# Optimization experiments

Hardware: AMD Instinct MI355X
Metric: run time of the kernel (lower is better)

The kernel has to match this reference:

```python
import jax, jax.numpy as jnp
import numpy as np

DT = 0.1  # fixed RK4 step size from the constructor

def setup_inputs() -> dict:
    key = jax.random.key(0)
    k1, k2, k3 = jax.random.split(key, 3)
    B, U, H = 65536, 128, 512
    x0 = jax.random.normal(k1, (B, U), dtype=jnp.float32)
    # small init so 20 unrolled RK4 steps stay numerically tame
    W1 = jax.random.normal(k2, (U, H), dtype=jnp.float32) * (0.5 / np.sqrt(U))
    b1 = jnp.zeros((H,), dtype=jnp.float32)
    W2 = jax.random.normal(k3, (H, U), dtype=jnp.float32) * (0.5 / np.sqrt(H))
    b2 = jnp.zeros((U,), dtype=jnp.float32)
    return {"x0": x0, "W1": W1, "b1": b1, "W2": W2, "b2": b2}

def _mlp(x, W1, b1, W2, b2):
    # vector field: Dense(512, relu) -> Dense(128); time-independent
    return jnp.maximum(x @ W1 + b1, 0.0) @ W2 + b2

def _rk4_integrate(x, n_steps, W1, b1, W2, b2):
    def step(x, _):
        k1 = _mlp(x, W1, b1, W2, b2)
        k2 = _mlp(x + 0.5 * DT * k1, W1, b1, W2, b2)
        k3 = _mlp(x + 0.5 * DT * k2, W1, b1, W2, b2)
        k4 = _mlp(x + DT * k3, W1, b1, W2, b2)
        return x + (DT / 6.0) * (k1 + 2.0 * k2 + 2.0 * k3 + k4), None
    x, _ = jax.lax.scan(step, x, None, length=n_steps)
    return x

def reference(x0, W1, b1, W2, b2):
    # phase 1: integrate t in [0, t1/2 = 1.0] -> 10 RK4 steps at dt=0.1
    x = _rk4_integrate(x0, 10, W1, b1, W2, b2)
    # phase 2: n=5 macro-steps of length (1.0 - 0.0)/5 = 0.2 -> 2 RK4 steps each
    def macro(x, _):
        x = _rk4_integrate(x, 2, W1, b1, W2, b2)
        return x, None
    x, _ = jax.lax.scan(macro, x, None, length=5)
    return x
```

## Files before the change

kernel.cpp:

```cpp
#include <hip/hip_runtime.h>
#include <stdint.h>


typedef _Float16 half8 __attribute__((ext_vector_type(8)));
typedef float f32x4 __attribute__((ext_vector_type(4)));
typedef __attribute__((address_space(3))) char lchar;
typedef __attribute__((address_space(1))) char gchar;

#define XSTR 136

static __device__ __forceinline__ void gload_lds16(const void* g, void* l) {
  __builtin_amdgcn_global_load_lds((const gchar*)g, (lchar*)l, 16, 0, 0);
}

static __device__ __forceinline__ unsigned short f2h(float x) {
  union { _Float16 h; unsigned short u; } cv;
  cv.h = (_Float16)x;
  return cv.u;
}
static __device__ __forceinline__ float h2f(unsigned short u) {
  union { unsigned short u; _Float16 h; } cv;
  cv.u = u;
  return (float)cv.h;
}
static __device__ __forceinline__ uint64_t pack4(float a, float b, float c, float d) {
  union { _Float16 h[4]; uint64_t q; } cv;
  cv.h[0] = (_Float16)a; cv.h[1] = (_Float16)b;
  cv.h[2] = (_Float16)c; cv.h[3] = (_Float16)d;
  return cv.q;
}

__global__ void pack_w(const float* __restrict__ W1, const float* __restrict__ W2,
                       unsigned short* __restrict__ wp) {
  int id = blockIdx.x * 256 + threadIdx.x;
  int lane = id & 63, fid = (id >> 6) & 255;
  int g = lane >> 4, lm = lane & 15;
  int c = fid >> 4, f = fid & 15;
  if (f < 8) {
    int T = f >> 2, ks = f & 3;
    int hid = c * 32 + T * 16 + lm;
#pragma unroll
    for (int j = 0; j < 8; ++j) {
      int kin = ks * 32 + g * 8 + j;
      wp[fid * 512 + lane * 8 + j] = f2h(W1[kin * 512 + hid]);
    }
  } else {
    int O = f - 8;
    int of = O * 16 + lm;
#pragma unroll
    for (int j = 0; j < 8; ++j) {
      int khl = (j < 4) ? (4 * g + j) : (16 + 4 * g + (j - 4));
      wp[fid * 512 + lane * 8 + j] = f2h(W2[(c * 32 + khl) * 128 + of]);
    }
  }
}

__global__ __launch_bounds__(512, 2) void node_rk4(
    const float* __restrict__ x0, const float* __restrict__ b1,
    const float* __restrict__ b2, const unsigned short* __restrict__ wp,
    float* __restrict__ out) {
  __shared__ char Wbuf[4][16384];
  __shared__ __align__(16) unsigned short xs[8][32][XSTR];
  __shared__ float b1s[512];
  __shared__ float b2s[128];

  const int tid = threadIdx.x;
  const int w = tid >> 6, lane = tid & 63;
  const int g = lane >> 4, lm = lane & 15;

  b1s[tid] = b1[tid];
  if (tid < 128) b2s[tid] = b2[tid];

  const int rbase = blockIdx.x * 256 + w * 32;
  f32x4 xa[2][8];
  ushort4 xbh[2][8];
#pragma unroll
  for (int mt = 0; mt < 2; ++mt)
#pragma unroll
    for (int O = 0; O < 8; ++O) {
      f32x4 v;
#pragma unroll
      for (int j = 0; j < 4; ++j)
        v[j] = x0[(rbase + mt * 16 + 4 * g + j) * 128 + O * 16 + lm];
      xa[mt][O] = v;
      ushort4 hq;
      hq.x = f2h(v[0]); hq.y = f2h(v[1]); hq.z = f2h(v[2]); hq.w = f2h(v[3]);
      xbh[mt][O] = hq;
      unsigned short* xr = &xs[w][mt * 16 + 4 * g][O * 16 + lm];
      xr[0] = hq.x; xr[XSTR] = hq.y; xr[2 * XSTR] = hq.z; xr[3 * XSTR] = hq.w;
    }

#pragma unroll
  for (int pc = 0; pc < 2; ++pc) {
    const char* src = (const char*)wp + pc * 16384;
#pragma unroll
    for (int q = 0; q < 2; ++q) {
      int seg = w * 2 + q;
      gload_lds16(src + seg * 1024 + lane * 16, Wbuf[pc] + seg * 1024);
    }
  }
  asm volatile("s_waitcnt vmcnt(2) lgkmcnt(0)" ::: "memory");
  __builtin_amdgcn_s_barrier();

#pragma unroll 1
  for (int it = 0; it < 80; ++it) {
    const int s = it & 3;
    const float wgt = (s == 0 || s == 3) ? (0.1f / 6.0f) : (0.1f / 3.0f);
    const float alph = (s < 2) ? 0.05f : 0.1f;

    half8 X1[2][4];
#pragma unroll
    for (int nt = 0; nt < 2; ++nt)
#pragma unroll
      for (int ks = 0; ks < 4; ++ks)
        X1[nt][ks] = *(const half8*)&xs[w][nt * 16 + lm][ks * 32 + g * 8];

    f32x4 yacc[2][8];
#pragma unroll
    for (int mt = 0; mt < 2; ++mt)
#pragma unroll
      for (int O = 0; O < 8; ++O) yacc[mt][O] = f32x4{0.f, 0.f, 0.f, 0.f};

    half8 hpk[2][2];

#pragma unroll
    for (int c = 0; c < 16; ++c) {
      {
        const int cn = (c + 2) & 15;
        char* buf = Wbuf[(c + 2) & 3];
        const char* src = (const char*)wp + cn * 16384;
#pragma unroll
        for (int q = 0; q < 2; ++q) {
          int seg = w * 2 + q;
          gload_lds16(src + seg * 1024 + lane * 16, buf + seg * 1024);
        }
      }

      __builtin_amdgcn_s_setprio(1);
      if (c > 0) {
        const char* Wp = Wbuf[(c + 3) & 3];
#pragma unroll
        for (int O = 0; O < 8; ++O) {
          half8 w2f = *(const half8*)(Wp + 8192 + O * 1024 + lane * 16);
          yacc[0][O] = __builtin_amdgcn_mfma_f32_16x16x32_f16(hpk[(c - 1) & 1][0], w2f,
                                                              yacc[0][O], 0, 0, 0);
          yacc[1][O] = __builtin_amdgcn_mfma_f32_16x16x32_f16(hpk[(c - 1) & 1][1], w2f,
                                                              yacc[1][O], 0, 0, 0);
        }
      }

      const char* Wb = Wbuf[c & 3];
      f32x4 hacc[2][2];
#pragma unroll
      for (int T = 0; T < 2; ++T)
#pragma unroll
        for (int nt = 0; nt < 2; ++nt) hacc[T][nt] = f32x4{0.f, 0.f, 0.f, 0.f};
#pragma unroll
      for (int T = 0; T < 2; ++T)
#pragma unroll
        for (int ks = 0; ks < 4; ++ks) {
          half8 wa = *(const half8*)(Wb + (T * 4 + ks) * 1024 + lane * 16);
          hacc[T][0] =
              __builtin_amdgcn_mfma_f32_16x16x32_f16(wa, X1[0][ks], hacc[T][0], 0, 0, 0);
          hacc[T][1] =
              __builtin_amdgcn_mfma_f32_16x16x32_f16(wa, X1[1][ks], hacc[T][1], 0, 0, 0);
        }
      __builtin_amdgcn_s_setprio(0);

      f32x4 bb0 = *(const f32x4*)&b1s[c * 32 + 4 * g];
      f32x4 bb1 = *(const f32x4*)&b1s[c * 32 + 16 + 4 * g];
#pragma unroll
      for (int nt = 0; nt < 2; ++nt) {
        union { uint64_t q[2]; half8 h; } u;
        u.q[0] = pack4(fmaxf(hacc[0][nt][0] + bb0[0], 0.f),
                       fmaxf(hacc[0][nt][1] + bb0[1], 0.f),
                       fmaxf(hacc[0][nt][2] + bb0[2], 0.f),
                       fmaxf(hacc[0][nt][3] + bb0[3], 0.f));
        u.q[1] = pack4(fmaxf(hacc[1][nt][0] + bb1[0], 0.f),
                       fmaxf(hacc[1][nt][1] + bb1[1], 0.f),
                       fmaxf(hacc[1][nt][2] + bb1[2], 0.f),
                       fmaxf(hacc[1][nt][3] + bb1[3], 0.f));
        hpk[c & 1][nt] = u.h;
      }

      asm volatile("s_waitcnt vmcnt(2)" ::: "memory");
      __builtin_amdgcn_s_barrier();
    }

    {
      const char* Wp = Wbuf[3];
#pragma unroll
      for (int O = 0; O < 8; ++O) {
        half8 w2f = *(const half8*)(Wp + 8192 + O * 1024 + lane * 16);
        yacc[0][O] =
            __builtin_amdgcn_mfma_f32_16x16x32_f16(hpk[1][0], w2f, yacc[0][O], 0, 0, 0);
        yacc[1][O] =
            __builtin_amdgcn_mfma_f32_16x16x32_f16(hpk[1][1], w2f, yacc[1][O], 0, 0, 0);
      }
    }

#pragma unroll
    for (int mt = 0; mt < 2; ++mt)
#pragma unroll
      for (int O = 0; O < 8; ++O) {
        float bb2 = b2s[O * 16 + lm];
        f32x4 k = yacc[mt][O];
#pragma unroll
        for (int j = 0; j < 4; ++j) k[j] += bb2;
        xa[mt][O] += wgt * k;
        ushort4 hq;
        if (s == 3) {
          f32x4 v = xa[mt][O];
          hq.x = f2h(v[0]); hq.y = f2h(v[1]); hq.z = f2h(v[2]); hq.w = f2h(v[3]);
          xbh[mt][O] = hq;
        } else {
          ushort4 xq = xbh[mt][O];
          hq.x = f2h(h2f(xq.x) + alph * k[0]);
          hq.y = f2h(h2f(xq.y) + alph * k[1]);
          hq.z = f2h(h2f(xq.z) + alph * k[2]);
          hq.w = f2h(h2f(xq.w) + alph * k[3]);
        }
        unsigned short* xr = &xs[w][mt * 16 + 4 * g][O * 16 + lm];
        xr[0] = hq.x; xr[XSTR] = hq.y; xr[2 * XSTR] = hq.z; xr[3 * XSTR] = hq.w;
      }
  }

#pragma unroll
  for (int mt = 0; mt < 2; ++mt)
#pragma unroll
    for (int O = 0; O < 8; ++O)
#pragma unroll
      for (int j = 0; j < 4; ++j)
        out[(rbase + mt * 16 + 4 * g + j) * 128 + O * 16 + lm] = xa[mt][O][j];
}

extern "C" void kernel_launch(void* const* d_in, const int* in_sizes, int n_in,
                              void* d_out, int out_size, void* d_ws, size_t ws_size,
                              hipStream_t stream) {
  const float* x0 = (const float*)d_in[0];
  const float* W1 = (const float*)d_in[1];
  const float* b1 = (const float*)d_in[2];
  const float* W2 = (const float*)d_in[3];
  const float* b2 = (const float*)d_in[4];
  float* out = (float*)d_out;

  unsigned short* wp = (unsigned short*)d_ws;

  pack_w<<<64, 256, 0, stream>>>(W1, W2, wp);
  node_rk4<<<256, 512, 0, stream>>>(x0, b1, b2, wp, out);
}
```

Before: 2.159 ms.

## Shrink blocks to 4 waves, split W1/W2 LDS buffers, swizzle x tile

Blocks shrink from 512 to 256 threads and the grid doubles to 512. The W1 and W2 halves of each chunk now get separate LDS ring buffers (2 for W1, 3 for W2), and the x staging tile uses an XOR-swizzled layout instead of padded rows. Bias b2 moves into registers. With a smaller LDS footprint and smaller blocks, more blocks can be resident and bank conflicts should drop, but each chunk now waits with vmcnt(0), which may expose load latency, and an extra barrier is added per RK stage.

After: 4.181 ms. 1.94x slower.

```diff
diff --git a/kernel.cpp b/kernel.cpp
--- a/kernel.cpp
+++ b/kernel.cpp
@@ -6,8 +6,6 @@
 typedef float f32x4 __attribute__((ext_vector_type(4)));
 typedef __attribute__((address_space(3))) char lchar;
 typedef __attribute__((address_space(1))) char gchar;
-
-#define XSTR 136
 
 static __device__ __forceinline__ void gload_lds16(const void* g, void* l) {
   __builtin_amdgcn_global_load_lds((const gchar*)g, (lchar*)l, 16, 0, 0);
@@ -28,6 +26,10 @@
   cv.h[0] = (_Float16)a; cv.h[1] = (_Float16)b;
   cv.h[2] = (_Float16)c; cv.h[3] = (_Float16)d;
   return cv.q;
+}
+
+static __device__ __forceinline__ int xs_off(int r, int f) {
+  return (r * 256 + f * 2) ^ ((r & 7) << 4);
 }
 
 __global__ void pack_w(const float* __restrict__ W1, const float* __restrict__ W2,
@@ -55,23 +57,27 @@
   }
 }
 
-__global__ __launch_bounds__(512, 2) void node_rk4(
+__global__ __launch_bounds__(256, 2) void node_rk4(
     const float* __restrict__ x0, const float* __restrict__ b1,
     const float* __restrict__ b2, const unsigned short* __restrict__ wp,
     float* __restrict__ out) {
-  __shared__ char Wbuf[4][16384];
-  __shared__ __align__(16) unsigned short xs[8][32][XSTR];
+  __shared__ char W1b[2][8192];
+  __shared__ char W2b[3][8192];
+  __shared__ __align__(16) char xsm[4][8192];
   __shared__ float b1s[512];
-  __shared__ float b2s[128];
 
   const int tid = threadIdx.x;
   const int w = tid >> 6, lane = tid & 63;
   const int g = lane >> 4, lm = lane & 15;
+  char* xw = xsm[w];
 
   b1s[tid] = b1[tid];
-  if (tid < 128) b2s[tid] = b2[tid];
-
-  const int rbase = blockIdx.x * 256 + w * 32;
+  b1s[tid + 256] = b1[tid + 256];
+  float b2v[8];
+#pragma unroll
+  for (int O = 0; O < 8; ++O) b2v[O] = b2[O * 16 + lm];
+
+  const int rbase = blockIdx.x * 128 + w * 32;
   f32x4 xa[2][8];
   ushort4 xbh[2][8];
 #pragma unroll
@@ -86,20 +92,18 @@
       ushort4 hq;
       hq.x = f2h(v[0]); hq.y = f2h(v[1]); hq.z = f2h(v[2]); hq.w = f2h(v[3]);
       xbh[mt][O] = hq;
-      unsigned short* xr = &xs[w][mt * 16 + 4 * g][O * 16 + lm];
-      xr[0] = hq.x; xr[XSTR] = hq.y; xr[2 * XSTR] = hq.z; xr[3 * XSTR] = hq.w;
-    }
-
-#pragma unroll
-  for (int pc = 0; pc < 2; ++pc) {
-    const char* src = (const char*)wp + pc * 16384;
-#pragma unroll
-    for (int q = 0; q < 2; ++q) {
-      int seg = w * 2 + q;
-      gload_lds16(src + seg * 1024 + lane * 16, Wbuf[pc] + seg * 1024);
-    }
+#pragma unroll
+      for (int j = 0; j < 4; ++j)
+        *(unsigned short*)(xw + xs_off(mt * 16 + 4 * g + j, O * 16 + lm)) =
+            (&hq.x)[j];
+    }
+
+#pragma unroll
+  for (int q = 0; q < 2; ++q) {
+    int seg = w * 2 + q;
+    gload_lds16((const char*)wp + seg * 1024 + lane * 16, W1b[0] + seg * 1024);
   }
-  asm volatile("s_waitcnt vmcnt(2) lgkmcnt(0)" ::: "memory");
+  asm volatile("s_waitcnt vmcnt(0) lgkmcnt(0)" ::: "memory");
   __builtin_amdgcn_s_barrier();
 
 #pragma unroll 1
@@ -113,7 +117,10 @@
     for (int nt = 0; nt < 2; ++nt)
 #pragma unroll
       for (int ks = 0; ks < 4; ++ks)
-        X1[nt][ks] = *(const half8*)&xs[w][nt * 16 + lm][ks * 32 + g * 8];
+        X1[nt][ks] =
+            *(const half8*)(xw + xs_off(nt * 16 + lm, ks * 32 + g * 8));
+
+    __builtin_amdgcn_s_barrier();
 
     f32x4 yacc[2][8];
 #pragma unroll
@@ -125,23 +132,40 @@
 
 #pragma unroll
     for (int c = 0; c < 16; ++c) {
-      {
-        const int cn = (c + 2) & 15;
-        char* buf = Wbuf[(c + 2) & 3];
-        const char* src = (const char*)wp + cn * 16384;
+      if (c == 0) {
 #pragma unroll
         for (int q = 0; q < 2; ++q) {
           int seg = w * 2 + q;
-          gload_lds16(src + seg * 1024 + lane * 16, buf + seg * 1024);
+          gload_lds16((const char*)wp + 16384 + seg * 1024 + lane * 16,
+                      W1b[1] + seg * 1024);
+          gload_lds16((const char*)wp + 8192 + seg * 1024 + lane * 16,
+                      W2b[0] + seg * 1024);
+          gload_lds16((const char*)wp + 16384 + 8192 + seg * 1024 + lane * 16,
+                      W2b[1] + seg * 1024);
+        }
+      } else if (c < 15) {
+        const char* src = (const char*)wp + (c + 1) * 16384;
+#pragma unroll
+        for (int q = 0; q < 2; ++q) {
+          int seg = w * 2 + q;
+          gload_lds16(src + seg * 1024 + lane * 16, W1b[(c + 1) & 1] + seg * 1024);
+          gload_lds16(src + 8192 + seg * 1024 + lane * 16,
+                      W2b[(c + 1) % 3] + seg * 1024);
+        }
+      } else {
+#pragma unroll
+        for (int q = 0; q < 2; ++q) {
+          int seg = w * 2 + q;
+          gload_lds16((const char*)wp + seg * 1024 + lane * 16, W1b[0] + seg * 1024);
         }
       }
 
       __builtin_amdgcn_s_setprio(1);
       if (c > 0) {
-        const char* Wp = Wbuf[(c + 3) & 3];
+        const char* Wp = W2b[(c - 1) % 3];
 #pragma unroll
         for (int O = 0; O < 8; ++O) {
-          half8 w2f = *(const half8*)(Wp + 8192 + O * 1024 + lane * 16);
+          half8 w2f = *(const half8*)(Wp + O * 1024 + lane * 16);
           yacc[0][O] = __builtin_amdgcn_mfma_f32_16x16x32_f16(hpk[(c - 1) & 1][0], w2f,
                                                               yacc[0][O], 0, 0, 0);
           yacc[1][O] = __builtin_amdgcn_mfma_f32_16x16x32_f16(hpk[(c - 1) & 1][1], w2f,
@@ -149,7 +173,7 @@
         }
       }
 
-      const char* Wb = Wbuf[c & 3];
+      const char* Wb = W1b[c & 1];
       f32x4 hacc[2][2];
 #pragma unroll
       for (int T = 0; T < 2; ++T)
@@ -183,15 +207,15 @@
         hpk[c & 1][nt] = u.h;
       }
 
-      asm volatile("s_waitcnt vmcnt(2)" ::: "memory");
+      asm volatile("s_waitcnt vmcnt(0)" ::: "memory");
       __builtin_amdgcn_s_barrier();
     }
 
     {
-      const char* Wp = Wbuf[3];
+      const char* Wp = W2b[0];
 #pragma unroll
       for (int O = 0; O < 8; ++O) {
-        half8 w2f = *(const half8*)(Wp + 8192 + O * 1024 + lane * 16);
+        half8 w2f = *(const half8*)(Wp + O * 1024 + lane * 16);
         yacc[0][O] =
             __builtin_amdgcn_mfma_f32_16x16x32_f16(hpk[1][0], w2f, yacc[0][O], 0, 0, 0);
         yacc[1][O] =
@@ -203,10 +227,9 @@
     for (int mt = 0; mt < 2; ++mt)
 #pragma unroll
       for (int O = 0; O < 8; ++O) {
-        float bb2 = b2s[O * 16 + lm];
         f32x4 k = yacc[mt][O];
 #pragma unroll
-        for (int j = 0; j < 4; ++j) k[j] += bb2;
+        for (int j = 0; j < 4; ++j) k[j] += b2v[O];
         xa[mt][O] += wgt * k;
         ushort4 hq;
         if (s == 3) {
@@ -220,8 +243,10 @@
           hq.z = f2h(h2f(xq.z) + alph * k[2]);
           hq.w = f2h(h2f(xq.w) + alph * k[3]);
         }
-        unsigned short* xr = &xs[w][mt * 16 + 4 * g][O * 16 + lm];
-        xr[0] = hq.x; xr[XSTR] = hq.y; xr[2 * XSTR] = hq.z; xr[3 * XSTR] = hq.w;
+#pragma unroll
+        for (int j = 0; j < 4; ++j)
+          *(unsigned short*)(xw + xs_off(mt * 16 + 4 * g + j, O * 16 + lm)) =
+              (&hq.x)[j];
       }
   }
 
@@ -247,5 +272,5 @@
   unsigned short* wp = (unsigned short*)d_ws;
 
   pack_w<<<64, 256, 0, stream>>>(W1, W2, wp);
-  node_rk4<<<256, 512, 0, stream>>>(x0, b1, b2, wp, out);
-}
+  node_rk4<<<512, 256, 0, stream>>>(x0, b1, b2, wp, out);
+}
```

## Split W1/W2 staging buffers and register-prefetch W1 fragments one chunk ahead

Applied to the files above, without the earlier changes.

Weights are repacked so that W1 and W2 chunks sit in separate contiguous regions and are staged into separate LDS ring buffers. W1 is fetched three chunks ahead and W2 two chunks ahead. W1 fragments for the next chunk are read from LDS into registers one iteration early, which reorders the loop so the first-layer MFMAs run before the second-layer ones. The aim is to hide LDS read latency behind MFMA work and to lengthen the global prefetch distance. In exchange it adds register pressure from the double-buffered W1 fragments, which could reduce occupancy at 2 waves per SIMD, and the vmcnt accounting becomes more delicate.

New measurement: 3.007 ms. 39.3% more time.

```diff
diff --git a/kernel.cpp b/kernel.cpp
--- a/kernel.cpp
+++ b/kernel.cpp
@@ -42,7 +42,7 @@
 #pragma unroll
     for (int j = 0; j < 8; ++j) {
       int kin = ks * 32 + g * 8 + j;
-      wp[fid * 512 + lane * 8 + j] = f2h(W1[kin * 512 + hid]);
+      wp[(c * 8 + f) * 512 + lane * 8 + j] = f2h(W1[kin * 512 + hid]);
     }
   } else {
     int O = f - 8;
@@ -50,7 +50,7 @@
 #pragma unroll
     for (int j = 0; j < 8; ++j) {
       int khl = (j < 4) ? (4 * g + j) : (16 + 4 * g + (j - 4));
-      wp[fid * 512 + lane * 8 + j] = f2h(W2[(c * 32 + khl) * 128 + of]);
+      wp[65536 + (c * 8 + O) * 512 + lane * 8 + j] = f2h(W2[(c * 32 + khl) * 128 + of]);
     }
   }
 }
@@ -59,7 +59,8 @@
     const float* __restrict__ x0, const float* __restrict__ b1,
     const float* __restrict__ b2, const unsigned short* __restrict__ wp,
     float* __restrict__ out) {
-  __shared__ char Wbuf[4][16384];
+  __shared__ char W1b[4][8192];
+  __shared__ char W2b[4][8192];
   __shared__ __align__(16) unsigned short xs[8][32][XSTR];
   __shared__ float b1s[512];
   __shared__ float b2s[128];
@@ -70,6 +71,9 @@
 
   b1s[tid] = b1[tid];
   if (tid < 128) b2s[tid] = b2[tid];
+
+  const char* w1g = (const char*)wp;
+  const char* w2g = (const char*)wp + 131072;
 
   const int rbase = blockIdx.x * 256 + w * 32;
   f32x4 xa[2][8];
@@ -90,17 +94,18 @@
       xr[0] = hq.x; xr[XSTR] = hq.y; xr[2 * XSTR] = hq.z; xr[3 * XSTR] = hq.w;
     }
 
-#pragma unroll
-  for (int pc = 0; pc < 2; ++pc) {
-    const char* src = (const char*)wp + pc * 16384;
-#pragma unroll
-    for (int q = 0; q < 2; ++q) {
-      int seg = w * 2 + q;
-      gload_lds16(src + seg * 1024 + lane * 16, Wbuf[pc] + seg * 1024);
-    }
-  }
+  gload_lds16(w1g + 0 * 8192 + w * 1024 + lane * 16, W1b[0] + w * 1024);
+  gload_lds16(w1g + 1 * 8192 + w * 1024 + lane * 16, W1b[1] + w * 1024);
+  gload_lds16(w2g + 0 * 8192 + w * 1024 + lane * 16, W2b[0] + w * 1024);
+  gload_lds16(w1g + 2 * 8192 + w * 1024 + lane * 16, W1b[2] + w * 1024);
+  gload_lds16(w2g + 1 * 8192 + w * 1024 + lane * 16, W2b[1] + w * 1024);
   asm volatile("s_waitcnt vmcnt(2) lgkmcnt(0)" ::: "memory");
   __builtin_amdgcn_s_barrier();
+
+  half8 w1r[2][8];
+#pragma unroll
+  for (int f = 0; f < 8; ++f)
+    w1r[0][f] = *(const half8*)(W1b[0] + f * 1024 + lane * 16);
 
 #pragma unroll 1
   for (int it = 0; it < 80; ++it) {
@@ -125,46 +130,44 @@
 
 #pragma unroll
     for (int c = 0; c < 16; ++c) {
-      {
-        const int cn = (c + 2) & 15;
-        char* buf = Wbuf[(c + 2) & 3];
-        const char* src = (const char*)wp + cn * 16384;
-#pragma unroll
-        for (int q = 0; q < 2; ++q) {
-          int seg = w * 2 + q;
-          gload_lds16(src + seg * 1024 + lane * 16, buf + seg * 1024);
+      gload_lds16(w1g + ((c + 3) & 15) * 8192 + w * 1024 + lane * 16,
+                  W1b[(c + 3) & 3] + w * 1024);
+      gload_lds16(w2g + ((c + 2) & 15) * 8192 + w * 1024 + lane * 16,
+                  W2b[(c + 2) & 3] + w * 1024);
+
+#pragma unroll
+      for (int f = 0; f < 8; ++f)
+        w1r[(c + 1) & 1][f] =
+            *(const half8*)(W1b[(c + 1) & 3] + f * 1024 + lane * 16);
+
+      __builtin_amdgcn_s_setprio(1);
+      f32x4 hacc[2][2];
+#pragma unroll
+      for (int T = 0; T < 2; ++T)
+#pragma unroll
+        for (int nt = 0; nt < 2; ++nt) hacc[T][nt] = f32x4{0.f, 0.f, 0.f, 0.f};
+#pragma unroll
+      for (int T = 0; T < 2; ++T)
+#pragma unroll
+        for (int ks = 0; ks < 4; ++ks) {
+          half8 wa = w1r[c & 1][T * 4 + ks];
+          hacc[T][0] =
+              __builtin_amdgcn_mfma_f32_16x16x32_f16(wa, X1[0][ks], hacc[T][0], 0, 0, 0);
+          hacc[T][1] =
+              __builtin_amdgcn_mfma_f32_16x16x32_f16(wa, X1[1][ks], hacc[T][1], 0, 0, 0);
         }
-      }
-
-      __builtin_amdgcn_s_setprio(1);
+
       if (c > 0) {
-        const char* Wp = Wbuf[(c + 3) & 3];
+        const char* Wp = W2b[(c - 1) & 3];
 #pragma unroll
         for (int O = 0; O < 8; ++O) {
-          half8 w2f = *(const half8*)(Wp + 8192 + O * 1024 + lane * 16);
+          half8 w2f = *(const half8*)(Wp + O * 1024 + lane * 16);
           yacc[0][O] = __builtin_amdgcn_mfma_f32_16x16x32_f16(hpk[(c - 1) & 1][0], w2f,
                                                               yacc[0][O], 0, 0, 0);
           yacc[1][O] = __builtin_amdgcn_mfma_f32_16x16x32_f16(hpk[(c - 1) & 1][1], w2f,
                                                               yacc[1][O], 0, 0, 0);
         }
       }
-
-      const char* Wb = Wbuf[c & 3];
-      f32x4 hacc[2][2];
-#pragma unroll
-      for (int T = 0; T < 2; ++T)
-#pragma unroll
-        for (int nt = 0; nt < 2; ++nt) hacc[T][nt] = f32x4{0.f, 0.f, 0.f, 0.f};
-#pragma unroll
-      for (int T = 0; T < 2; ++T)
-#pragma unroll
-        for (int ks = 0; ks < 4; ++ks) {
-          half8 wa = *(const half8*)(Wb + (T * 4 + ks) * 1024 + lane * 16);
-          hacc[T][0] =
-              __builtin_amdgcn_mfma_f32_16x16x32_f16(wa, X1[0][ks], hacc[T][0], 0, 0, 0);
-          hacc[T][1] =
-              __builtin_amdgcn_mfma_f32_16x16x32_f16(wa, X1[1][ks], hacc[T][1], 0, 0, 0);
-        }
       __builtin_amdgcn_s_setprio(0);
 
       f32x4 bb0 = *(const f32x4*)&b1s[c * 32 + 4 * g];
@@ -183,15 +186,15 @@
         hpk[c & 1][nt] = u.h;
       }
 
-      asm volatile("s_waitcnt vmcnt(2)" ::: "memory");
+      asm volatile("s_waitcnt vmcnt(3)" ::: "memory");
       __builtin_amdgcn_s_barrier();
     }
 
     {
-      const char* Wp = Wbuf[3];
+      const char* Wp = W2b[3];
 #pragma unroll
       for (int O = 0; O < 8; ++O) {
-        half8 w2f = *(const half8*)(Wp + 8192 + O * 1024 + lane * 16);
+        half8 w2f = *(const half8*)(Wp + O * 1024 + lane * 16);
         yacc[0][O] =
             __builtin_amdgcn_mfma_f32_16x16x32_f16(hpk[1][0], w2f, yacc[0][O], 0, 0, 0);
         yacc[1][O] =
```

## Deepen weight ring to 8 chunks, barrier every 4, shrink x transpose buffer

Applied to the files above, without the earlier changes.

Grows the LDS weight ring from 4 to 8 chunks and prefetches 4 chunks at once, so the block barrier and vmcnt wait happen once per 4 hidden chunks instead of every chunk. The second GEMM now runs inside the same chunk rather than being software-pipelined one chunk behind. The per-wave fp16 state transpose goes through a small 32x80-byte bounce buffer, processed in 4 slices, instead of a full 32x136 tile, and b2 is held in registers. The aim is fewer barriers and less LDS traffic; the cost is double the weight LDS footprint, which may reduce occupancy, and less overlap between the two GEMMs.

New measurement: 4.298 ms. 1.99x slower.

```diff
diff --git a/kernel.cpp b/kernel.cpp
--- a/kernel.cpp
+++ b/kernel.cpp
@@ -6,8 +6,6 @@
 typedef float f32x4 __attribute__((ext_vector_type(4)));
 typedef __attribute__((address_space(3))) char lchar;
 typedef __attribute__((address_space(1))) char gchar;
-
-#define XSTR 136
 
 static __device__ __forceinline__ void gload_lds16(const void* g, void* l) {
   __builtin_amdgcn_global_load_lds((const gchar*)g, (lchar*)l, 16, 0, 0);
@@ -59,17 +57,19 @@
     const float* __restrict__ x0, const float* __restrict__ b1,
     const float* __restrict__ b2, const unsigned short* __restrict__ wp,
     float* __restrict__ out) {
-  __shared__ char Wbuf[4][16384];
-  __shared__ __align__(16) unsigned short xs[8][32][XSTR];
+  __shared__ char Wring[8][16384];
+  __shared__ __align__(16) char bnc[8][2560];
   __shared__ float b1s[512];
-  __shared__ float b2s[128];
 
   const int tid = threadIdx.x;
   const int w = tid >> 6, lane = tid & 63;
   const int g = lane >> 4, lm = lane & 15;
+  char* bw = bnc[w];
 
   b1s[tid] = b1[tid];
-  if (tid < 128) b2s[tid] = b2[tid];
+  float b2v[8];
+#pragma unroll
+  for (int O = 0; O < 8; ++O) b2v[O] = b2[O * 16 + lm];
 
   const int rbase = blockIdx.x * 256 + w * 32;
   f32x4 xa[2][8];
@@ -86,21 +86,28 @@
       ushort4 hq;
       hq.x = f2h(v[0]); hq.y = f2h(v[1]); hq.z = f2h(v[2]); hq.w = f2h(v[3]);
       xbh[mt][O] = hq;
-      unsigned short* xr = &xs[w][mt * 16 + 4 * g][O * 16 + lm];
-      xr[0] = hq.x; xr[XSTR] = hq.y; xr[2 * XSTR] = hq.z; xr[3 * XSTR] = hq.w;
-    }
-
-#pragma unroll
-  for (int pc = 0; pc < 2; ++pc) {
+    }
+
+  half8 X1[2][4];
+#pragma unroll
+  for (int nt = 0; nt < 2; ++nt)
+#pragma unroll
+    for (int ks = 0; ks < 4; ++ks) {
+      const float* xr = &x0[(rbase + nt * 16 + lm) * 128 + ks * 32 + g * 8];
+      f32x4 a = *(const f32x4*)xr;
+      f32x4 b = *(const f32x4*)(xr + 4);
+      union { uint64_t q[2]; half8 h; } u;
+      u.q[0] = pack4(a[0], a[1], a[2], a[3]);
+      u.q[1] = pack4(b[0], b[1], b[2], b[3]);
+      X1[nt][ks] = u.h;
+    }
+
+#pragma unroll
+  for (int pc = 0; pc < 4; ++pc) {
     const char* src = (const char*)wp + pc * 16384;
-#pragma unroll
-    for (int q = 0; q < 2; ++q) {
-      int seg = w * 2 + q;
-      gload_lds16(src + seg * 1024 + lane * 16, Wbuf[pc] + seg * 1024);
-    }
+    gload_lds16(src + w * 1024 + lane * 16, Wring[pc] + w * 1024);
+    gload_lds16(src + 8192 + w * 1024 + lane * 16, Wring[pc] + 8192 + w * 1024);
   }
-  asm volatile("s_waitcnt vmcnt(2) lgkmcnt(0)" ::: "memory");
-  __builtin_amdgcn_s_barrier();
 
 #pragma unroll 1
   for (int it = 0; it < 80; ++it) {
@@ -108,48 +115,30 @@
     const float wgt = (s == 0 || s == 3) ? (0.1f / 6.0f) : (0.1f / 3.0f);
     const float alph = (s < 2) ? 0.05f : 0.1f;
 
-    half8 X1[2][4];
-#pragma unroll
-    for (int nt = 0; nt < 2; ++nt)
-#pragma unroll
-      for (int ks = 0; ks < 4; ++ks)
-        X1[nt][ks] = *(const half8*)&xs[w][nt * 16 + lm][ks * 32 + g * 8];
-
     f32x4 yacc[2][8];
 #pragma unroll
     for (int mt = 0; mt < 2; ++mt)
 #pragma unroll
       for (int O = 0; O < 8; ++O) yacc[mt][O] = f32x4{0.f, 0.f, 0.f, 0.f};
 
-    half8 hpk[2][2];
-
 #pragma unroll
     for (int c = 0; c < 16; ++c) {
-      {
-        const int cn = (c + 2) & 15;
-        char* buf = Wbuf[(c + 2) & 3];
-        const char* src = (const char*)wp + cn * 16384;
-#pragma unroll
-        for (int q = 0; q < 2; ++q) {
-          int seg = w * 2 + q;
-          gload_lds16(src + seg * 1024 + lane * 16, buf + seg * 1024);
+      if ((c & 3) == 0) {
+        asm volatile("s_waitcnt vmcnt(0)" ::: "memory");
+        __builtin_amdgcn_s_barrier();
+#pragma unroll
+        for (int d = 0; d < 4; ++d) {
+          const int cn = (c + 4 + d) & 15;
+          char* dst = Wring[(c + 4 + d) & 7];
+          const char* src = (const char*)wp + cn * 16384;
+          gload_lds16(src + w * 1024 + lane * 16, dst + w * 1024);
+          gload_lds16(src + 8192 + w * 1024 + lane * 16, dst + 8192 + w * 1024);
         }
       }
 
+      const char* Wb = Wring[c & 7];
+
       __builtin_amdgcn_s_setprio(1);
-      if (c > 0) {
-        const char* Wp = Wbuf[(c + 3) & 3];
-#pragma unroll
-        for (int O = 0; O < 8; ++O) {
-          half8 w2f = *(const half8*)(Wp + 8192 + O * 1024 + lane * 16);
-          yacc[0][O] = __builtin_amdgcn_mfma_f32_16x16x32_f16(hpk[(c - 1) & 1][0], w2f,
-                                                              yacc[0][O], 0, 0, 0);
-          yacc[1][O] = __builtin_amdgcn_mfma_f32_16x16x32_f16(hpk[(c - 1) & 1][1], w2f,
-                                                              yacc[1][O], 0, 0, 0);
-        }
-      }
-
-      const char* Wb = Wbuf[c & 3];
       f32x4 hacc[2][2];
 #pragma unroll
       for (int T = 0; T < 2; ++T)
@@ -169,60 +158,84 @@
 
       f32x4 bb0 = *(const f32x4*)&b1s[c * 32 + 4 * g];
       f32x4 bb1 = *(const f32x4*)&b1s[c * 32 + 16 + 4 * g];
-#pragma unroll
-      for (int nt = 0; nt < 2; ++nt) {
+      half8 hpk0, hpk1;
+      {
         union { uint64_t q[2]; half8 h; } u;
-        u.q[0] = pack4(fmaxf(hacc[0][nt][0] + bb0[0], 0.f),
-                       fmaxf(hacc[0][nt][1] + bb0[1], 0.f),
-                       fmaxf(hacc[0][nt][2] + bb0[2], 0.f),
-                       fmaxf(hacc[0][nt][3] + bb0[3], 0.f));
-        u.q[1] = pack4(fmaxf(hacc[1][nt][0] + bb1[0], 0.f),
-                       fmaxf(hacc[1][nt][1] + bb1[1], 0.f),
-                       fmaxf(hacc[1][nt][2] + bb1[2], 0.f),
-                       fmaxf(hacc[1][nt][3] + bb1[3], 0.f));
-        hpk[c & 1][nt] = u.h;
-      }
-
-      asm volatile("s_waitcnt vmcnt(2)" ::: "memory");
-      __builtin_amdgcn_s_barrier();
-    }
-
-    {
-      const char* Wp = Wbuf[3];
+        u.q[0] = pack4(fmaxf(hacc[0][0][0] + bb0[0], 0.f),
+                       fmaxf(hacc[0][0][1] + bb0[1], 0.f),
+                       fmaxf(hacc[0][0][2] + bb0[2], 0.f),
+                       fmaxf(hacc[0][0][3] + bb0[3], 0.f));
+        u.q[1] = pack4(fmaxf(hacc[1][0][0] + bb1[0], 0.f),
+                       fmaxf(hacc[1][0][1] + bb1[1], 0.f),
+                       fmaxf(hacc[1][0][2] + bb1[2], 0.f),
+                       fmaxf(hacc[1][0][3] + bb1[3], 0.f));
+        hpk0 = u.h;
+        u.q[0] = pack4(fmaxf(hacc[0][1][0] + bb0[0], 0.f),
+                       fmaxf(hacc[0][1][1] + bb0[1], 0.f),
+                       fmaxf(hacc[0][1][2] + bb0[2], 0.f),
+                       fmaxf(hacc[0][1][3] + bb0[3], 0.f));
+        u.q[1] = pack4(fmaxf(hacc[1][1][0] + bb1[0], 0.f),
+                       fmaxf(hacc[1][1][1] + bb1[1], 0.f),
+                       fmaxf(hacc[1][1][2] + bb1[2], 0.f),
+                       fmaxf(hacc[1][1][3] + bb1[3], 0.f));
+        hpk1 = u.h;
+      }
+
+      __builtin_amdgcn_s_setprio(1);
 #pragma unroll
       for (int O = 0; O < 8; ++O) {
-        half8 w2f = *(const half8*)(Wp + 8192 + O * 1024 + lane * 16);
-        yacc[0][O] =
-            __builtin_amdgcn_mfma_f32_16x16x32_f16(hpk[1][0], w2f, yacc[0][O], 0, 0, 0);
-        yacc[1][O] =
-            __builtin_amdgcn_mfma_f32_16x16x32_f16(hpk[1][1], w2f, yacc[1][O], 0, 0, 0);
-      }
-    }
-
-#pragma unroll
-    for (int mt = 0; mt < 2; ++mt)
-#pragma unroll
-      for (int O = 0; O < 8; ++O) {
-        float bb2 = b2s[O * 16 + lm];
-        f32x4 k = yacc[mt][O];
-#pragma unroll
-        for (int j = 0; j < 4; ++j) k[j] += bb2;
-        xa[mt][O] += wgt * k;
-        ushort4 hq;
-        if (s == 3) {
-          f32x4 v = xa[mt][O];
-          hq.x = f2h(v[0]); hq.y = f2h(v[1]); hq.z = f2h(v[2]); hq.w = f2h(v[3]);
-          xbh[mt][O] = hq;
-        } else {
-          ushort4 xq = xbh[mt][O];
-          hq.x = f2h(h2f(xq.x) + alph * k[0]);
-          hq.y = f2h(h2f(xq.y) + alph * k[1]);
-          hq.z = f2h(h2f(xq.z) + alph * k[2]);
-          hq.w = f2h(h2f(xq.w) + alph * k[3]);
+        half8 w2f = *(const half8*)(Wb + 8192 + O * 1024 + lane * 16);
+        yacc[0][O] = __builtin_amdgcn_mfma_f32_16x16x32_f16(hpk0, w2f, yacc[0][O], 0, 0, 0);
+        yacc[1][O] = __builtin_amdgcn_mfma_f32_16x16x32_f16(hpk1, w2f, yacc[1][O], 0, 0, 0);
+      }
+      __builtin_amdgcn_s_setprio(0);
+    }
+
+    if (it < 79) {
+#pragma unroll
+      for (int ks = 0; ks < 4; ++ks) {
+#pragma unroll
+        for (int mt = 0; mt < 2; ++mt)
+#pragma unroll
+          for (int Oh = 0; Oh < 2; ++Oh) {
+            const int O = 2 * ks + Oh;
+            f32x4 k = yacc[mt][O];
+#pragma unroll
+            for (int j = 0; j < 4; ++j) k[j] += b2v[O];
+            xa[mt][O] += wgt * k;
+            ushort4 hq;
+            if (s == 3) {
+              f32x4 v = xa[mt][O];
+              hq.x = f2h(v[0]); hq.y = f2h(v[1]); hq.z = f2h(v[2]); hq.w = f2h(v[3]);
+              xbh[mt][O] = hq;
+            } else {
+              ushort4 xq = xbh[mt][O];
+              hq.x = f2h(h2f(xq.x) + alph * k[0]);
+              hq.y = f2h(h2f(xq.y) + alph * k[1]);
+              hq.z = f2h(h2f(xq.z) + alph * k[2]);
+              hq.w = f2h(h2f(xq.w) + alph * k[3]);
+            }
+            char* base = bw + (mt * 16 + 4 * g) * 80 + (Oh * 16 + lm) * 2;
+            *(unsigned short*)(base) = hq.x;
+            *(unsigned short*)(base + 80) = hq.y;
+            *(unsigned short*)(base + 160) = hq.z;
+            *(unsigned short*)(base + 240) = hq.w;
+          }
+#pragma unroll
+        for (int nt = 0; nt < 2; ++nt)
+          X1[nt][ks] = *(const half8*)(bw + (nt * 16 + lm) * 80 + g * 16);
+      }
+    } else {
+#pragma unroll
+      for (int mt = 0; mt < 2; ++mt)
+#pragma unroll
+        for (int O = 0; O < 8; ++O) {
+          f32x4 k = yacc[mt][O];
+#pragma unroll
+          for (int j = 0; j < 4; ++j) k[j] += b2v[O];
+          xa[mt][O] += wgt * k;
         }
-        unsigned short* xr = &xs[w][mt * 16 + 4 * g][O * 16 + lm];
-        xr[0] = hq.x; xr[XSTR] = hq.y; xr[2 * XSTR] = hq.z; xr[3 * XSTR] = hq.w;
-      }
+    }
   }
 
 #pragma unroll
```
